# Kernel optimization log

Hardware: AMD Instinct MI355X
Metric: run time of the kernel (lower is better)

## Reference

```python
import jax, jax.numpy as jnp
import numpy as np

N_CLASS = 8192
FEAT_DIM = 1024
BATCH = 1024
PROTO_M = 0.95
TEMP = 0.1
BASE_TEMP = 0.1
EPS = 1e-12  # F.normalize eps


def setup_inputs() -> dict:
    key = jax.random.key(0)
    k1, k2, k3 = jax.random.split(key, 3)
    features = jax.random.normal(k1, (BATCH, FEAT_DIM), dtype=jnp.float32)
    labels = jax.random.randint(k2, (BATCH,), 0, N_CLASS)
    prototypes = jax.random.normal(k3, (N_CLASS, FEAT_DIM), dtype=jnp.float32)
    # init_class_prototypes ends with F.normalize(prototypes, dim=1)
    prototypes = prototypes / jnp.maximum(
        jnp.linalg.norm(prototypes, axis=1, keepdims=True), EPS)
    return {"features": features, "labels": labels, "prototypes": prototypes}


def _ema_update(prototypes, features, labels):
    # Sequential per-sample EMA scatter update (order matters for repeated labels),
    # expressed as a lax.scan over the batch.
    def step(protos, fl):
        f, l = fl
        row = protos[l] * PROTO_M + f * (1.0 - PROTO_M)
        row = row / jnp.maximum(jnp.linalg.norm(row), EPS)  # F.normalize(dim=0)
        return protos.at[l].set(row), None

    protos, _ = jax.lax.scan(step, prototypes, (features, labels))
    return protos


def reference(features, labels, prototypes):
    protos = _ema_update(prototypes, features, labels)  # [C, D]
    logits = jnp.matmul(protos, protos.T) / TEMP        # [C, C]
    exp_l = jnp.exp(logits)
    # mask = off-diagonal ones (labels are arange(n_class)), so the masked sum
    # is the row sum minus the diagonal; mask.sum(1) == n_class - 1 (never NaN).
    sum_neg = exp_l.sum(axis=1) - jnp.diagonal(exp_l)   # [C]
    mean_prob_neg = jnp.log(sum_neg / jnp.float32(N_CLASS - 1))
    loss = (TEMP / BASE_TEMP) * jnp.mean(mean_prob_neg)
    return loss
```

## Files before the change

### kernel.cpp

```cpp
#include <hip/hip_runtime.h>
#include <math.h>

#define C 8192
#define D 1024
#define BATCH 1024
#define PM 0.95f
#define PMC 0.05f
#define INVT_I8 (10.0f / 16129.0f)

typedef unsigned char u8;
typedef __attribute__((ext_vector_type(16))) int i32x16;
typedef __attribute__((ext_vector_type(4))) int i32x4;

#define GLOBAL_AS(p) ((const __attribute__((address_space(1))) void*)(p))
#define LDS_AS(p) ((__attribute__((address_space(3))) void*)(p))

__global__ __launch_bounds__(256) void ema_split_kernel(const float* __restrict__ feat,
                                                        const int* __restrict__ labels,
                                                        const float* __restrict__ protos,
                                                        u8* __restrict__ P8,
                                                        float* __restrict__ rowsum,
                                                        float* __restrict__ out) {
    __shared__ int sl[BATCH];
    __shared__ unsigned int sq[64][16][4];
    const int t = threadIdx.x, w = t >> 6, lane = t & 63;
    const int cb = blockIdx.x * 16;

    if (blockIdx.x < 32) rowsum[blockIdx.x * 256 + t] = 0.0f;
    if (blockIdx.x == 0 && t == 0) out[0] = 0.0f;

    for (int i = t; i < BATCH; i += 256) sl[i] = labels[i];
    __syncthreads();

    for (int i = 0; i < 4; ++i) {
        const int c = cb + w * 4 + i;

        float4 v[4];
        #pragma unroll
        for (int s = 0; s < 4; ++s)
            v[s] = *(const float4*)(protos + (size_t)c * D + s * 256 + lane * 4);

        for (int base = 0; base < BATCH; base += 64) {
            unsigned long long mask = __ballot(sl[base + lane] == c);
            while (mask) {
                const int b = __ffsll((long long)mask) - 1;
                mask &= mask - 1;
                const int idx = base + b;
                float ss = 0.0f;
                #pragma unroll
                for (int s = 0; s < 4; ++s) {
                    const float4 f = *(const float4*)(feat + (size_t)idx * D + s * 256 + lane * 4);
                    v[s].x = v[s].x * PM + f.x * PMC;
                    v[s].y = v[s].y * PM + f.y * PMC;
                    v[s].z = v[s].z * PM + f.z * PMC;
                    v[s].w = v[s].w * PM + f.w * PMC;
                    ss += v[s].x * v[s].x + v[s].y * v[s].y + v[s].z * v[s].z + v[s].w * v[s].w;
                }
                #pragma unroll
                for (int off = 32; off > 0; off >>= 1) ss += __shfl_xor(ss, off);
                const float inv = 1.0f / fmaxf(sqrtf(ss), 1e-12f);
                #pragma unroll
                for (int s = 0; s < 4; ++s) {
                    v[s].x *= inv; v[s].y *= inv; v[s].z *= inv; v[s].w *= inv;
                }
            }
        }

        #pragma unroll
        for (int s = 0; s < 4; ++s) {
            const int qx = __float2int_rn(v[s].x * 127.0f);
            const int qy = __float2int_rn(v[s].y * 127.0f);
            const int qz = __float2int_rn(v[s].z * 127.0f);
            const int qw = __float2int_rn(v[s].w * 127.0f);
            const unsigned int pk = (qx & 0xFF) | ((qy & 0xFF) << 8) |
                                    ((qz & 0xFF) << 16) | ((unsigned int)(qw & 0xFF) << 24);
            sq[s * 16 + (lane >> 2)][w * 4 + i][lane & 3] = pk;
        }
    }
    __syncthreads();

    u8* base2 = P8 + (size_t)(cb >> 5) * 32768 + (cb & 31) * 16;
    #pragma unroll
    for (int it = 0; it < 4; ++it) {
        const int slot = it * 256 + t;
        const int pp16 = slot >> 4, cls = slot & 15;
        uint4 val;
        val.x = sq[pp16][cls][0]; val.y = sq[pp16][cls][1];
        val.z = sq[pp16][cls][2]; val.w = sq[pp16][cls][3];
        *(uint4*)(base2 + (pp16 >> 1) * 1024 + (pp16 & 1) * 512 + cls * 16) = val;
    }
}

__global__ __launch_bounds__(256, 4) void gram8_kernel(const u8* __restrict__ P8,
                                                       float* __restrict__ rowsum) {
    __shared__ u8 lds[5][8192];
    const int t = threadIdx.x, w = t >> 6, lane = t & 63;

    int mm = blockIdx.x >> 3;
    const int r = blockIdx.x & 7;
    int bi = 0;
    #pragma unroll
    for (int s = 0; s < 8; ++s) {
        const int strip = (s & 1) ? ((s >> 1) * 16 + 15 - r) : ((s >> 1) * 16 + r);
        const int n = 64 - strip;
        if (mm < n) { bi = strip; break; }
        mm -= n;
    }
    const int bj = bi + mm;
    const bool diag = (bi == bj);

    const u8* gsrcA = P8 + (size_t)(bi * 4 + w) * 32768 + lane * 16;
    const u8* gsrcB = P8 + (size_t)(bj * 4 + w) * 32768 + lane * 16;
    const int ldsA = w * 1024, ldsB = 4096 + w * 1024;

    const int qi = w >> 1, qj = w & 1;
    const int aT0 = qi * 2048;
    const int bT0 = 4096 + qj * 2048;
    const int alof = (lane >> 5) * 512 + (lane & 31) * 16;

    i32x16 acc[2][2];
    #pragma unroll
    for (int a = 0; a < 2; ++a)
        #pragma unroll
        for (int b = 0; b < 2; ++b)
            #pragma unroll
            for (int e = 0; e < 16; ++e) acc[a][b][e] = 0;

    i32x4 fa[2][2], fb[2][2];

#define STAGE(KC, BUF)                                                         \
    __builtin_amdgcn_global_load_lds(GLOBAL_AS(gsrcA + (size_t)(KC) * 1024),   \
                                     LDS_AS(&lds[BUF][ldsA]), 16, 0, 0);       \
    __builtin_amdgcn_global_load_lds(GLOBAL_AS(gsrcB + (size_t)(KC) * 1024),   \
                                     LDS_AS(&lds[BUF][ldsB]), 16, 0, 0);

#define PF(SET, BUF)                                                           \
    fa[SET][0] = *(const i32x4*)&lds[BUF][aT0 + alof];                         \
    fa[SET][1] = *(const i32x4*)&lds[BUF][aT0 + 1024 + alof];                  \
    fb[SET][0] = *(const i32x4*)&lds[BUF][bT0 + alof];                         \
    fb[SET][1] = *(const i32x4*)&lds[BUF][bT0 + 1024 + alof];

#define MFMA4(SET)                                                             \
    acc[0][0] = __builtin_amdgcn_mfma_i32_32x32x32_i8(fa[SET][0], fb[SET][0], acc[0][0], 0, 0, 0); \
    acc[0][1] = __builtin_amdgcn_mfma_i32_32x32x32_i8(fa[SET][0], fb[SET][1], acc[0][1], 0, 0, 0); \
    acc[1][0] = __builtin_amdgcn_mfma_i32_32x32x32_i8(fa[SET][1], fb[SET][0], acc[1][0], 0, 0, 0); \
    acc[1][1] = __builtin_amdgcn_mfma_i32_32x32x32_i8(fa[SET][1], fb[SET][1], acc[1][1], 0, 0, 0);

#define WAITV(N) asm volatile("s_waitcnt vmcnt(" #N ")" ::: "memory")

    STAGE(0, 0); STAGE(1, 1); STAGE(2, 2); STAGE(3, 3);
    WAITV(4);
    __builtin_amdgcn_s_barrier();
    PF(0, 0);

    int cbuf = 0;
    for (int kc = 0; kc < 28; ++kc) {
        const int sb = (cbuf >= 1) ? cbuf - 1 : 4;
        STAGE(kc + 4, sb);
        const int nb = (cbuf == 4) ? 0 : cbuf + 1;
        PF((kc + 1) & 1, nb);
        MFMA4(kc & 1);
        WAITV(4);
        __builtin_amdgcn_s_barrier();
        cbuf = nb;
    }
    PF(1, 4);
    MFMA4(0);
    WAITV(2); __builtin_amdgcn_s_barrier();
    PF(0, 0);
    MFMA4(1);
    WAITV(0); __builtin_amdgcn_s_barrier();
    PF(1, 1);
    MFMA4(0);
    MFMA4(1);

    __syncthreads();
    float* rpart = (float*)&lds[0][0];
    float* cpart = (float*)&lds[0][512];
    if (t < 128) { rpart[t] = 0.0f; cpart[t] = 0.0f; }
    __syncthreads();
    const int half = lane >> 5, col = lane & 31;
    float csum[2] = {0.0f, 0.0f};
    #pragma unroll
    for (int ti = 0; ti < 2; ++ti) {
        float rs[16];
        #pragma unroll
        for (int reg = 0; reg < 16; ++reg) rs[reg] = 0.0f;
        #pragma unroll
        for (int tj = 0; tj < 2; ++tj) {
            const int lj = qj * 64 + tj * 32 + col;
            #pragma unroll
            for (int reg = 0; reg < 16; ++reg) {
                const int li = qi * 64 + ti * 32 + (reg & 3) + 8 * (reg >> 2) + 4 * half;
                float e = __expf((float)acc[ti][tj][reg] * INVT_I8);
                if (diag && li >= lj) e = 0.0f;
                rs[reg] += e;
                csum[tj] += e;
            }
        }
        #pragma unroll
        for (int reg = 0; reg < 16; ++reg) {
            float v = rs[reg];
            v += __shfl_xor(v, 1); v += __shfl_xor(v, 2); v += __shfl_xor(v, 4);
            v += __shfl_xor(v, 8); v += __shfl_xor(v, 16);
            if (col == 0)
                atomicAdd(&rpart[qi * 64 + ti * 32 + (reg & 3) + 8 * (reg >> 2) + 4 * half], v);
        }
    }
    #pragma unroll
    for (int tj = 0; tj < 2; ++tj) {
        float v = csum[tj];
        v += __shfl_xor(v, 32);
        if (half == 0) atomicAdd(&cpart[qj * 64 + tj * 32 + col], v);
    }
    __syncthreads();
    if (t < 128) atomicAdd(&rowsum[bi * 128 + t], rpart[t]);
    else         atomicAdd(&rowsum[bj * 128 + (t - 128)], cpart[t - 128]);
}

__global__ __launch_bounds__(256) void final2_kernel(const float* __restrict__ rowsum,
                                                     float* __restrict__ out) {
    __shared__ float red[4];
    const int t = threadIdx.x;
    const int i = blockIdx.x * 256 + t;
    float v = logf(rowsum[i] * (1.0f / (float)(C - 1)));
    #pragma unroll
    for (int off = 32; off > 0; off >>= 1) v += __shfl_down(v, off);
    if ((t & 63) == 0) red[t >> 6] = v;
    __syncthreads();
    if (t == 0)
        atomicAdd(out, (red[0] + red[1] + red[2] + red[3]) * (1.0f / (float)C));
}

extern "C" void kernel_launch(void* const* d_in, const int* in_sizes, int n_in,
                              void* d_out, int out_size, void* d_ws, size_t ws_size,
                              hipStream_t stream) {
    const float* feat = (const float*)d_in[0];
    const int* labels = (const int*)d_in[1];
    const float* protos = (const float*)d_in[2];
    float* out = (float*)d_out;
    float* rowsum = (float*)d_ws;
    u8* P8 = (u8*)((char*)d_ws + 32768);

    ema_split_kernel<<<C / 16, 256, 0, stream>>>(feat, labels, protos, P8, rowsum, out);
    gram8_kernel<<<2080, 256, 0, stream>>>(P8, rowsum);
    final2_kernel<<<C / 256, 256, 0, stream>>>(rowsum, out);
}
```

Measured before the change: 147.7 us.

## Load int8 MFMA operands directly from global memory, dropping LDS staging pipeline

Replaces the 5-buffer LDS staging (global_load_lds plus barriers) in the int8 Gram kernel with direct per-lane 16-byte global loads into registers, double-buffered across the unrolled k loop. This removes the LDS footprint, the barriers and the vmcnt waits, which could allow more blocks per CU. In exchange each wave fetches its own operands, so data shared between waves is loaded twice from L2/global and the prefetch distance shrinks to one step, risking exposed memory latency.

```diff
diff --git a/kernel.cpp b/kernel.cpp
--- a/kernel.cpp
+++ b/kernel.cpp
@@ -11,9 +11,6 @@
 typedef unsigned char u8;
 typedef __attribute__((ext_vector_type(16))) int i32x16;
 typedef __attribute__((ext_vector_type(4))) int i32x4;
-
-#define GLOBAL_AS(p) ((const __attribute__((address_space(1))) void*)(p))
-#define LDS_AS(p) ((__attribute__((address_space(3))) void*)(p))
 
 __global__ __launch_bounds__(256) void ema_split_kernel(const float* __restrict__ feat,
                                                         const int* __restrict__ labels,
@@ -93,7 +90,7 @@
 
 __global__ __launch_bounds__(256, 4) void gram8_kernel(const u8* __restrict__ P8,
                                                        float* __restrict__ rowsum) {
-    __shared__ u8 lds[5][8192];
+    __shared__ float epart[256];
     const int t = threadIdx.x, w = t >> 6, lane = t & 63;
 
     int mm = blockIdx.x >> 3;
@@ -109,14 +106,13 @@
     const int bj = bi + mm;
     const bool diag = (bi == bj);
 
-    const u8* gsrcA = P8 + (size_t)(bi * 4 + w) * 32768 + lane * 16;
-    const u8* gsrcB = P8 + (size_t)(bj * 4 + w) * 32768 + lane * 16;
-    const int ldsA = w * 1024, ldsB = 4096 + w * 1024;
-
     const int qi = w >> 1, qj = w & 1;
-    const int aT0 = qi * 2048;
-    const int bT0 = 4096 + qj * 2048;
     const int alof = (lane >> 5) * 512 + (lane & 31) * 16;
+
+    const u8* pA0 = P8 + (size_t)(bi * 4 + 2 * qi) * 32768 + alof;
+    const u8* pA1 = P8 + (size_t)(bi * 4 + 2 * qi + 1) * 32768 + alof;
+    const u8* pB0 = P8 + (size_t)(bj * 4 + 2 * qj) * 32768 + alof;
+    const u8* pB1 = P8 + (size_t)(bj * 4 + 2 * qj + 1) * 32768 + alof;
 
     i32x16 acc[2][2];
     #pragma unroll
@@ -128,17 +124,11 @@
 
     i32x4 fa[2][2], fb[2][2];
 
-#define STAGE(KC, BUF)                                                         \
-    __builtin_amdgcn_global_load_lds(GLOBAL_AS(gsrcA + (size_t)(KC) * 1024),   \
-                                     LDS_AS(&lds[BUF][ldsA]), 16, 0, 0);       \
-    __builtin_amdgcn_global_load_lds(GLOBAL_AS(gsrcB + (size_t)(KC) * 1024),   \
-                                     LDS_AS(&lds[BUF][ldsB]), 16, 0, 0);
-
-#define PF(SET, BUF)                                                           \
-    fa[SET][0] = *(const i32x4*)&lds[BUF][aT0 + alof];                         \
-    fa[SET][1] = *(const i32x4*)&lds[BUF][aT0 + 1024 + alof];                  \
-    fb[SET][0] = *(const i32x4*)&lds[BUF][bT0 + alof];                         \
-    fb[SET][1] = *(const i32x4*)&lds[BUF][bT0 + 1024 + alof];
+#define LOADSET(SET, KC)                                                       \
+    fa[SET][0] = *(const i32x4*)(pA0 + (size_t)(KC) * 1024);                   \
+    fa[SET][1] = *(const i32x4*)(pA1 + (size_t)(KC) * 1024);                   \
+    fb[SET][0] = *(const i32x4*)(pB0 + (size_t)(KC) * 1024);                   \
+    fb[SET][1] = *(const i32x4*)(pB1 + (size_t)(KC) * 1024);
 
 #define MFMA4(SET)                                                             \
     acc[0][0] = __builtin_amdgcn_mfma_i32_32x32x32_i8(fa[SET][0], fb[SET][0], acc[0][0], 0, 0, 0); \
@@ -146,38 +136,17 @@
     acc[1][0] = __builtin_amdgcn_mfma_i32_32x32x32_i8(fa[SET][1], fb[SET][0], acc[1][0], 0, 0, 0); \
     acc[1][1] = __builtin_amdgcn_mfma_i32_32x32x32_i8(fa[SET][1], fb[SET][1], acc[1][1], 0, 0, 0);
 
-#define WAITV(N) asm volatile("s_waitcnt vmcnt(" #N ")" ::: "memory")
-
-    STAGE(0, 0); STAGE(1, 1); STAGE(2, 2); STAGE(3, 3);
-    WAITV(4);
-    __builtin_amdgcn_s_barrier();
-    PF(0, 0);
-
-    int cbuf = 0;
-    for (int kc = 0; kc < 28; ++kc) {
-        const int sb = (cbuf >= 1) ? cbuf - 1 : 4;
-        STAGE(kc + 4, sb);
-        const int nb = (cbuf == 4) ? 0 : cbuf + 1;
-        PF((kc + 1) & 1, nb);
+    LOADSET(0, 0);
+    #pragma unroll
+    for (int kc = 0; kc < 31; ++kc) {
+        LOADSET((kc + 1) & 1, kc + 1);
         MFMA4(kc & 1);
-        WAITV(4);
-        __builtin_amdgcn_s_barrier();
-        cbuf = nb;
-    }
-    PF(1, 4);
-    MFMA4(0);
-    WAITV(2); __builtin_amdgcn_s_barrier();
-    PF(0, 0);
+    }
     MFMA4(1);
-    WAITV(0); __builtin_amdgcn_s_barrier();
-    PF(1, 1);
-    MFMA4(0);
-    MFMA4(1);
-
-    __syncthreads();
-    float* rpart = (float*)&lds[0][0];
-    float* cpart = (float*)&lds[0][512];
-    if (t < 128) { rpart[t] = 0.0f; cpart[t] = 0.0f; }
+
+    float* rpart = &epart[0];
+    float* cpart = &epart[128];
+    epart[t & 255] = 0.0f;
     __syncthreads();
     const int half = lane >> 5, col = lane & 31;
     float csum[2] = {0.0f, 0.0f};
```

New measurement: 156.2 us. 5.8% more time.
